# Performance work log

Measured on AMD Instinct MI355X. Metric: run time of the kernel, lower is better.

## Reference

```python
import jax, jax.numpy as jnp
import numpy as np

H, DQ, DK, DV, DM = 16, 64, 64, 64, 1024
NEG = -1.0e12


def setup_inputs() -> dict:
    key = jax.random.key(0)
    ks = jax.random.split(key, 16)
    B, S = 4, 1024
    s = 0.02
    inp = {
        "query": jax.random.normal(ks[0], (B, S, DM), jnp.float32),
        "key": jax.random.normal(ks[1], (B, S, DM), jnp.float32),
        "value": jax.random.normal(ks[2], (B, S, DM), jnp.float32),
        "mask": jax.random.randint(ks[3], (B, S), 0, 2, jnp.int32),
        "Wq": jax.random.normal(ks[4], (H * DQ, DM), jnp.float32) * s,
        "bq": jnp.zeros((H * DQ,), jnp.float32),
        "Wk": jax.random.normal(ks[5], (H * DK, DM), jnp.float32) * s,
        "bk": jnp.zeros((H * DK,), jnp.float32),
        "Wv": jax.random.normal(ks[6], (H * DV, DM), jnp.float32) * s,
        "bv": jnp.zeros((H * DV,), jnp.float32),
        "Wo": jax.random.normal(ks[7], (DM, H * DV), jnp.float32) * s,
        "bo": jnp.zeros((DM,), jnp.float32),
        "ln_g": jnp.ones((DM,), jnp.float32),
        "ln_b": jnp.zeros((DM,), jnp.float32),
    }
    return inp


def _attention(query, key, value, mask, Wq, bq, Wk, bk, Wv, bv, Wo, bo, ln_g, ln_b):
    B, qL, _ = query.shape
    kL = key.shape[1]
    mf = mask.astype(jnp.float32)  # [B, kL] ; 1 = masked token
    # padding mask broadcast over query rows, then self-attn: masked query rows fully masked
    m = jnp.broadcast_to(mf[:, None, :], (B, qL, kL))
    m = jnp.where(mf[:, :, None] > 0, 1.0, m)  # [B, q, k]

    def proj(x, W, b, d):
        # [B,S,DM] -> [H,B,S,d]
        return (x @ W.T + b).reshape(B, -1, H, d).transpose(2, 0, 1, 3)

    q = proj(query, Wq, bq, DQ)
    k = proj(key, Wk, bk, DK)
    v = proj(value, Wv, bv, DV)

    scores = jnp.einsum("hbqd,hbkd->hbqk", q, k) / np.float32(np.sqrt(DK))
    fut = jnp.triu(jnp.ones((qL, kL), jnp.float32), k=1)  # [q,k] future mask
    scores = scores + m[None] * NEG + fut[None, None] * NEG
    attn = jax.nn.softmax(scores, axis=-1)
    attn = attn * (1.0 - m[None]) * (1.0 - fut[None, None])

    out = jnp.einsum("hbqk,hbkd->hbqd", attn, v)  # [H,B,q,DV]
    out = out.transpose(1, 2, 0, 3).reshape(B, qL, H * DV)
    out = out @ Wo.T + bo + query  # residual
    mu = jnp.mean(out, axis=-1, keepdims=True)
    var = jnp.mean(jnp.square(out - mu), axis=-1, keepdims=True)
    out = (out - mu) * jax.lax.rsqrt(var + 1e-12) * ln_g + ln_b
    return out, attn.reshape(H * B, qL, kL)


def reference(query, key, value, mask, Wq, bq, Wk, bk, Wv, bv, Wo, bo, ln_g, ln_b):
    return _attention(query, key, value, mask, Wq, bq, Wk, bk, Wv, bv, Wo, bo, ln_g, ln_b)
```

## Files before the change

kernel.cpp:

```cpp
#include <hip/hip_runtime.h>
#include <hip/hip_bf16.h>

typedef __attribute__((ext_vector_type(4))) float f32x4;
typedef __attribute__((ext_vector_type(4))) float fv4;
typedef __attribute__((ext_vector_type(8))) short bf16x8;
typedef __attribute__((ext_vector_type(4))) short bf16x4;

#define DEVI __device__ __forceinline__

constexpr int BATCH = 4, SEQ = 1024, NH = 16, HD = 64, DM_ = 1024;
constexpr int NTOK = BATCH * SEQ;

DEVI unsigned short f2bf(float f) {
  union { float f; unsigned u; } v; v.f = f;
  unsigned r = v.u + 0x7FFFu + ((v.u >> 16) & 1u);
  return (unsigned short)(r >> 16);
}

DEVI int swz64(int row, int col) {
  int byte = (row * 64 + col) * 2;
  byte ^= (row & 7) << 4;
  return byte >> 1;
}

DEVI void gld_lds16(const unsigned short* g, unsigned short* l) {
  __builtin_amdgcn_global_load_lds(
      (const __attribute__((address_space(1))) unsigned int*)g,
      (__attribute__((address_space(3))) unsigned int*)l, 16, 0, 0);
}

__global__ __launch_bounds__(256) void k_cvt(
    const float* __restrict__ q, const float* __restrict__ k,
    const float* __restrict__ v,
    const float* __restrict__ wq, const float* __restrict__ wk,
    const float* __restrict__ wv, const float* __restrict__ wo,
    unsigned short* __restrict__ Xb, unsigned short* __restrict__ Wb)
{
  const int a = blockIdx.y;
  const float* src;
  unsigned short* dst;
  int n;
  if (a < 3) {
    src = (a == 0) ? q : (a == 1) ? k : v;
    dst = Xb + (size_t)a * NTOK * DM_;
    n = NTOK * DM_;
  } else {
    src = (a == 3) ? wq : (a == 4) ? wk : (a == 5) ? wv : wo;
    dst = Wb + (size_t)(a - 3) * DM_ * DM_;
    n = DM_ * DM_;
  }
  const int idx = (blockIdx.x * 256 + threadIdx.x) * 8;
  if (idx >= n) return;
  fv4 v0 = *(const fv4*)(src + idx);
  fv4 v1 = *(const fv4*)(src + idx + 4);
  bf16x8 o;
  o[0] = (short)f2bf(v0[0]); o[1] = (short)f2bf(v0[1]);
  o[2] = (short)f2bf(v0[2]); o[3] = (short)f2bf(v0[3]);
  o[4] = (short)f2bf(v1[0]); o[5] = (short)f2bf(v1[1]);
  o[6] = (short)f2bf(v1[2]); o[7] = (short)f2bf(v1[3]);
  *(bf16x8*)(dst + idx) = o;
}

__global__ __launch_bounds__(256, 3) void k_proj(
    const unsigned short* __restrict__ Xb, const unsigned short* __restrict__ Wb,
    const float* __restrict__ bq, const float* __restrict__ bk,
    const float* __restrict__ bv,
    unsigned short* __restrict__ qo, unsigned short* __restrict__ ko,
    unsigned short* __restrict__ vTo)
{
  const int lid = blockIdx.x;
  const int wg = (lid & 7) * 96 + (lid >> 3);
  const int m0 = (wg & 31) * 128;
  const int o0g = (wg >> 5) * 128;
  const int z = o0g >> 10;
  const int o0 = o0g & 1023;

  const unsigned short* X = Xb + (size_t)z * NTOK * DM_;
  const float* bias = (z == 0) ? bq : (z == 1) ? bk : bv;

  __shared__ __align__(16) unsigned short Al[128 * 64];
  __shared__ __align__(16) unsigned short Bl[128 * 64];

  const int tid = threadIdx.x;
  const int lane = tid & 63;
  const int w = tid >> 6;
  const int wm = w & 1, wn = w >> 1;
  const int l15 = lane & 15, lg = lane >> 4;

  const int rseg = lane >> 3;
  const int cg = (lane & 7) ^ rseg;

  f32x4 acc[4][4];
#pragma unroll
  for (int i = 0; i < 4; ++i)
#pragma unroll
    for (int j = 0; j < 4; ++j) acc[i][j] = f32x4{0.f, 0.f, 0.f, 0.f};

  for (int kt = 0; kt < 16; ++kt) {
    const int k0 = kt * 64;
    __syncthreads();
#pragma unroll
    for (int i = 0; i < 4; ++i) {
      const int seg = w * 4 + i;
      const int row = seg * 8 + rseg;
      gld_lds16(X + (size_t)(m0 + row) * DM_ + k0 + cg * 8, &Al[seg * 512]);
      gld_lds16(Wb + (size_t)(o0g + row) * DM_ + k0 + cg * 8, &Bl[seg * 512]);
    }
    __syncthreads();
#pragma unroll
    for (int kk = 0; kk < 2; ++kk) {
      bf16x8 af[4], bfm[4];
#pragma unroll
      for (int m = 0; m < 4; ++m)
        af[m] = *(const bf16x8*)&Al[swz64(wm * 64 + m * 16 + l15, kk * 32 + lg * 8)];
#pragma unroll
      for (int n = 0; n < 4; ++n)
        bfm[n] = *(const bf16x8*)&Bl[swz64(wn * 64 + n * 16 + l15, kk * 32 + lg * 8)];
#pragma unroll
      for (int m = 0; m < 4; ++m)
#pragma unroll
        for (int n = 0; n < 4; ++n)
          acc[m][n] = __builtin_amdgcn_mfma_f32_16x16x32_bf16(af[m], bfm[n], acc[m][n], 0, 0, 0);
    }
  }

#pragma unroll
  for (int n = 0; n < 4; ++n) {
    const int colg = o0 + wn * 64 + n * 16 + l15;
    const float bb = bias[colg];
#pragma unroll
    for (int m = 0; m < 4; ++m) {
      const int rbase = m0 + wm * 64 + m * 16 + lg * 4;
      if (z == 2) {
        bf16x4 pv;
#pragma unroll
        for (int j = 0; j < 4; ++j) pv[j] = (short)f2bf(acc[m][n][j] + bb);
        *(bf16x4*)&vTo[((size_t)(rbase >> 10) * 1024 + colg) * 1024 + (rbase & 1023)] = pv;
      } else {
        unsigned short* Y = (z == 0) ? qo : ko;
        const float sc = (z == 0) ? 0.125f : 1.f;
#pragma unroll
        for (int j = 0; j < 4; ++j)
          Y[(size_t)(rbase + j) * DM_ + colg] = f2bf((acc[m][n][j] + bb) * sc);
      }
    }
  }
}

__global__ __launch_bounds__(512, 2) void k_attn_pv(
    const unsigned short* __restrict__ qb, const unsigned short* __restrict__ kb,
    const unsigned short* __restrict__ vT, const int* __restrict__ mask,
    float* __restrict__ attn, unsigned short* __restrict__ Ob)
{
  const int tid = threadIdx.x;
  const int lane = tid & 63;
  const int w = tid >> 6;
  const int l15 = lane & 15, lg = lane >> 4;
  const int hb = blockIdx.y;
  const int h = hb >> 2, b = hb & 3;
  const int bx = blockIdx.x;
  const int q0 = bx * 32;

  __shared__ __align__(16) unsigned short Pl[32 * 1024];
  __shared__ float red[8][2][16];

  int qglob[2];
  qglob[0] = q0 + l15;
  qglob[1] = q0 + 16 + l15;

  bf16x8 qf[2][2];
#pragma unroll
  for (int g = 0; g < 2; ++g) {
    const unsigned short* qp = qb + (size_t)(b * SEQ + qglob[g]) * DM_ + h * HD + lg * 8;
    qf[g][0] = *(const bf16x8*)qp;
    qf[g][1] = *(const bf16x8*)(qp + 32);
  }
  int qm[2];
  qm[0] = mask[b * SEQ + qglob[0]];
  qm[1] = mask[b * SEQ + qglob[1]];

  const int tt = 2 * bx + 1;
  const int ni = (tt >= w) ? ((tt - w) >> 3) + 1 : 0;

  bf16x8 kf[8][2];
#pragma unroll
  for (int i = 0; i < 8; ++i) {
    if (i < ni) {
      const int krow = (w + 8 * i) * 16 + l15;
      const unsigned short* kp = kb + (size_t)(b * SEQ + krow) * DM_ + h * HD + lg * 8;
      kf[i][0] = *(const bf16x8*)kp;
      kf[i][1] = *(const bf16x8*)(kp + 32);
    }
  }

  f32x4 acc[8][2];
#pragma unroll
  for (int i = 0; i < 8; ++i)
#pragma unroll
    for (int g = 0; g < 2; ++g) acc[i][g] = f32x4{0.f, 0.f, 0.f, 0.f};

#pragma unroll
  for (int i = 0; i < 8; ++i) {
    if (i < ni) {
#pragma unroll
      for (int g = 0; g < 2; ++g) {
        acc[i][g] = __builtin_amdgcn_mfma_f32_16x16x32_bf16(kf[i][0], qf[g][0], acc[i][g], 0, 0, 0);
        acc[i][g] = __builtin_amdgcn_mfma_f32_16x16x32_bf16(kf[i][1], qf[g][1], acc[i][g], 0, 0, 0);
      }
    }
  }

  unsigned kvb = 0;
#pragma unroll
  for (int i = 0; i < 8; ++i) {
    if (i < ni) {
      const int kbase = (w + 8 * i) * 16 + lg * 4;
      int4 mv = *(const int4*)&mask[b * SEQ + kbase];
      if (mv.x == 0) kvb |= 1u << (i * 4 + 0);
      if (mv.y == 0) kvb |= 1u << (i * 4 + 1);
      if (mv.z == 0) kvb |= 1u << (i * 4 + 2);
      if (mv.w == 0) kvb |= 1u << (i * 4 + 3);
    }
  }

  float s[2] = {0.f, 0.f};
#pragma unroll
  for (int i = 0; i < 8; ++i) {
    if (i < ni) {
      const int kbase = (w + 8 * i) * 16 + lg * 4;
#pragma unroll
      for (int j = 0; j < 4; ++j) {
        const bool kok = (kvb >> (i * 4 + j)) & 1u;
#pragma unroll
        for (int g = 0; g < 2; ++g) {
          const bool vld = kok && (qm[g] == 0) && (kbase + j <= qglob[g]);
          const float p = vld ? __expf(acc[i][g][j]) : 0.f;
          acc[i][g][j] = p;
          s[g] += p;
        }
      }
    }
  }
#pragma unroll
  for (int g = 0; g < 2; ++g) {
    s[g] += __shfl_xor(s[g], 16, 64);
    s[g] += __shfl_xor(s[g], 32, 64);
  }
  if (lane < 16) { red[w][0][l15] = s[0]; red[w][1][l15] = s[1]; }
  __syncthreads();
  float rinv[2];
#pragma unroll
  for (int g = 0; g < 2; ++g) {
    float sm = 0.f;
#pragma unroll
    for (int ww = 0; ww < 8; ++ww) sm += red[ww][g][l15];
    rinv[g] = (sm > 0.f) ? (1.f / sm) : 0.f;
  }

#pragma unroll
  for (int i = 0; i < 8; ++i) {
    const int kbase = (w + 8 * i) * 16 + lg * 4;
#pragma unroll
    for (int g = 0; g < 2; ++g) {
      float* ap = attn + (size_t)hb * SEQ * SEQ + (size_t)qglob[g] * SEQ;
      fv4 st = fv4{0.f, 0.f, 0.f, 0.f};
      bf16x4 pb = bf16x4{0, 0, 0, 0};
      if (i < ni) {
#pragma unroll
        for (int j = 0; j < 4; ++j) {
          st[j] = acc[i][g][j] * rinv[g];
          pb[j] = (short)f2bf(acc[i][g][j]);
        }
      }
      __builtin_nontemporal_store(st, (fv4*)&ap[kbase]);
      const int row = g * 16 + l15;
      const int pbyte = ((row * 1024 + kbase) * 2) ^ ((l15 & 7) << 4);
      *(bf16x4*)((char*)Pl + pbyte) = pb;
    }
  }
  __syncthreads();

  const int dt = w & 3, g = w >> 2;
  const int prow = g * 16 + l15;
  f32x4 o = f32x4{0.f, 0.f, 0.f, 0.f};
  const unsigned short* vr = vT + (size_t)(b * 1024 + h * HD + dt * 16 + l15) * 1024;
#pragma unroll 4
  for (int kt = 0; kt <= bx; ++kt) {
    const int k0 = kt * 32 + lg * 8;
    bf16x8 vf = *(const bf16x8*)(vr + k0);
    const int pbyte = ((prow * 1024 + k0) * 2) ^ ((l15 & 7) << 4);
    bf16x8 pf = *(const bf16x8*)((const char*)Pl + pbyte);
    o = __builtin_amdgcn_mfma_f32_16x16x32_bf16(vf, pf, o, 0, 0, 0);
  }

  bf16x4 ob;
#pragma unroll
  for (int j = 0; j < 4; ++j) ob[j] = (short)f2bf(o[j] * rinv[g]);
  *(bf16x4*)&Ob[(size_t)(b * SEQ + q0 + prow) * DM_ + h * HD + dt * 16 + lg * 4] = ob;
}

__global__ __launch_bounds__(256) void k_oproj(
    const unsigned short* __restrict__ Ob, const unsigned short* __restrict__ Wb,
    const float* __restrict__ bo, const float* __restrict__ query,
    float* __restrict__ preln)
{
  const unsigned short* W = Wb + (size_t)3 * DM_ * DM_;

  __shared__ __align__(16) unsigned short Al[2][64 * 64];
  __shared__ __align__(16) unsigned short Bl[2][128 * 64];

  const int tid = threadIdx.x;
  const int lane = tid & 63;
  const int w = tid >> 6;
  const int wm = w & 1, wn = w >> 1;
  const int l15 = lane & 15, lg = lane >> 4;
  const int m0 = blockIdx.x * 64;
  const int o0 = blockIdx.y * 128;

  const int rseg = lane >> 3;
  const int cg = (lane & 7) ^ rseg;

  f32x4 acc[2][4];
#pragma unroll
  for (int i = 0; i < 2; ++i)
#pragma unroll
    for (int j = 0; j < 4; ++j) acc[i][j] = f32x4{0.f, 0.f, 0.f, 0.f};

#define OPROJ_STAGE(nb, kt)                                                    \
  {                                                                            \
    const int k0_ = (kt) * 64;                                                 \
    _Pragma("unroll") for (int i = 0; i < 2; ++i) {                            \
      const int seg = w * 2 + i;                                               \
      gld_lds16(Ob + (size_t)(m0 + seg * 8 + rseg) * DM_ + k0_ + cg * 8,       \
                &Al[nb][seg * 512]);                                           \
    }                                                                          \
    _Pragma("unroll") for (int i = 0; i < 4; ++i) {                            \
      const int seg = w * 4 + i;                                               \
      gld_lds16(W + (size_t)(o0 + seg * 8 + rseg) * DM_ + k0_ + cg * 8,        \
                &Bl[nb][seg * 512]);                                           \
    }                                                                          \
  }

  OPROJ_STAGE(0, 0);
  __syncthreads();

  for (int kt = 0; kt < 16; ++kt) {
    const int cur = kt & 1;
    if (kt < 15) OPROJ_STAGE(cur ^ 1, kt + 1);
#pragma unroll
    for (int kk = 0; kk < 2; ++kk) {
      bf16x8 af[2], bfm[4];
#pragma unroll
      for (int m = 0; m < 2; ++m)
        af[m] = *(const bf16x8*)&Al[cur][swz64(wm * 32 + m * 16 + l15, kk * 32 + lg * 8)];
#pragma unroll
      for (int n = 0; n < 4; ++n)
        bfm[n] = *(const bf16x8*)&Bl[cur][swz64(wn * 64 + n * 16 + l15, kk * 32 + lg * 8)];
#pragma unroll
      for (int m = 0; m < 2; ++m)
#pragma unroll
        for (int n = 0; n < 4; ++n)
          acc[m][n] = __builtin_amdgcn_mfma_f32_16x16x32_bf16(af[m], bfm[n], acc[m][n], 0, 0, 0);
    }
    __syncthreads();
  }

#pragma unroll
  for (int n = 0; n < 4; ++n) {
    const int oc = o0 + wn * 64 + n * 16 + l15;
    const float bb = bo[oc];
#pragma unroll
    for (int m = 0; m < 2; ++m) {
      const int rbase = m0 + wm * 32 + m * 16 + lg * 4;
#pragma unroll
      for (int j = 0; j < 4; ++j) {
        const size_t idx = (size_t)(rbase + j) * DM_ + oc;
        preln[idx] = acc[m][n][j] + bb + query[idx];
      }
    }
  }
}

__global__ __launch_bounds__(256) void k_ln(
    const float* __restrict__ x, const float* __restrict__ g,
    const float* __restrict__ bta, float* __restrict__ out)
{
  const int row = blockIdx.x;
  const int tid = threadIdx.x;
  const float* xr = x + (size_t)row * DM_;
  fv4 v = *(const fv4*)(xr + tid * 4);
  float s = v[0] + v[1] + v[2] + v[3];
  float s2 = v[0] * v[0] + v[1] * v[1] + v[2] * v[2] + v[3] * v[3];
#pragma unroll
  for (int off = 1; off < 64; off <<= 1) {
    s += __shfl_xor(s, off, 64);
    s2 += __shfl_xor(s2, off, 64);
  }
  __shared__ float rs[2][4];
  const int w = tid >> 6;
  if ((tid & 63) == 0) { rs[0][w] = s; rs[1][w] = s2; }
  __syncthreads();
  s = rs[0][0] + rs[0][1] + rs[0][2] + rs[0][3];
  s2 = rs[1][0] + rs[1][1] + rs[1][2] + rs[1][3];
  const float mu = s * (1.f / 1024.f);
  const float var = s2 * (1.f / 1024.f) - mu * mu;
  const float rstd = rsqrtf(var + 1e-12f);
  fv4 gg = *(const fv4*)(g + tid * 4);
  fv4 bb = *(const fv4*)(bta + tid * 4);
  fv4 o;
#pragma unroll
  for (int j = 0; j < 4; ++j) o[j] = (v[j] - mu) * rstd * gg[j] + bb[j];
  *(fv4*)(out + (size_t)row * DM_ + tid * 4) = o;
}

extern "C" void kernel_launch(void* const* d_in, const int* in_sizes, int n_in,
                              void* d_out, int out_size, void* d_ws, size_t ws_size,
                              hipStream_t stream) {
  const float* query = (const float*)d_in[0];
  const float* key   = (const float*)d_in[1];
  const float* value = (const float*)d_in[2];
  const int*   mask  = (const int*)d_in[3];
  const float* Wq = (const float*)d_in[4];
  const float* bq = (const float*)d_in[5];
  const float* Wk = (const float*)d_in[6];
  const float* bk = (const float*)d_in[7];
  const float* Wv = (const float*)d_in[8];
  const float* bv = (const float*)d_in[9];
  const float* Wo = (const float*)d_in[10];
  const float* bo = (const float*)d_in[11];
  const float* ln_g = (const float*)d_in[12];
  const float* ln_b = (const float*)d_in[13];

  float* out  = (float*)d_out;
  float* attn = out + (size_t)NTOK * DM_;

  char* ws = (char*)d_ws;
  unsigned short* Xb = (unsigned short*)ws;
  unsigned short* Wb = Xb + (size_t)3 * NTOK * DM_;
  unsigned short* qb = Wb + (size_t)4 * DM_ * DM_;
  unsigned short* kb = qb + (size_t)NTOK * DM_;
  unsigned short* vT = kb + (size_t)NTOK * DM_;
  unsigned short* Ob = vT + (size_t)NTOK * DM_;
  float* preln = (float*)ws;

  k_cvt<<<dim3(2048, 7), 256, 0, stream>>>(query, key, value, Wq, Wk, Wv, Wo,
                                           Xb, Wb);
  k_proj<<<768, 256, 0, stream>>>(Xb, Wb, bq, bk, bv, qb, kb, vT);
  k_attn_pv<<<dim3(32, 64), 512, 0, stream>>>(qb, kb, vT, mask, attn, Ob);
  k_oproj<<<dim3(64, 8), 256, 0, stream>>>(Ob, Wb, bo, query, preln);
  k_ln<<<4096, 256, 0, stream>>>(preln, ln_g, ln_b, out);
}
```

Before: 499.1 us.

## Defer attn probability stores past PV matmul, split accumulators, raise MFMA priority

```diff
diff --git a/kernel.cpp b/kernel.cpp
--- a/kernel.cpp
+++ b/kernel.cpp
@@ -199,6 +199,7 @@
 #pragma unroll
     for (int g = 0; g < 2; ++g) acc[i][g] = f32x4{0.f, 0.f, 0.f, 0.f};
 
+  __builtin_amdgcn_s_setprio(1);
 #pragma unroll
   for (int i = 0; i < 8; ++i) {
     if (i < ni) {
@@ -209,6 +210,7 @@
       }
     }
   }
+  __builtin_amdgcn_s_setprio(0);
 
   unsigned kvb = 0;
 #pragma unroll
@@ -247,32 +249,17 @@
     s[g] += __shfl_xor(s[g], 32, 64);
   }
   if (lane < 16) { red[w][0][l15] = s[0]; red[w][1][l15] = s[1]; }
-  __syncthreads();
-  float rinv[2];
-#pragma unroll
-  for (int g = 0; g < 2; ++g) {
-    float sm = 0.f;
-#pragma unroll
-    for (int ww = 0; ww < 8; ++ww) sm += red[ww][g][l15];
-    rinv[g] = (sm > 0.f) ? (1.f / sm) : 0.f;
-  }
 
 #pragma unroll
   for (int i = 0; i < 8; ++i) {
     const int kbase = (w + 8 * i) * 16 + lg * 4;
 #pragma unroll
     for (int g = 0; g < 2; ++g) {
-      float* ap = attn + (size_t)hb * SEQ * SEQ + (size_t)qglob[g] * SEQ;
-      fv4 st = fv4{0.f, 0.f, 0.f, 0.f};
       bf16x4 pb = bf16x4{0, 0, 0, 0};
       if (i < ni) {
 #pragma unroll
-        for (int j = 0; j < 4; ++j) {
-          st[j] = acc[i][g][j] * rinv[g];
-          pb[j] = (short)f2bf(acc[i][g][j]);
-        }
-      }
-      __builtin_nontemporal_store(st, (fv4*)&ap[kbase]);
+        for (int j = 0; j < 4; ++j) pb[j] = (short)f2bf(acc[i][g][j]);
+      }
       const int row = g * 16 + l15;
       const int pbyte = ((row * 1024 + kbase) * 2) ^ ((l15 & 7) << 4);
       *(bf16x4*)((char*)Pl + pbyte) = pb;
@@ -280,23 +267,59 @@
   }
   __syncthreads();
 
+  float rinv[2];
+#pragma unroll
+  for (int g = 0; g < 2; ++g) {
+    float sm = 0.f;
+#pragma unroll
+    for (int ww = 0; ww < 8; ++ww) sm += red[ww][g][l15];
+    rinv[g] = (sm > 0.f) ? (1.f / sm) : 0.f;
+  }
+
   const int dt = w & 3, g = w >> 2;
   const int prow = g * 16 + l15;
-  f32x4 o = f32x4{0.f, 0.f, 0.f, 0.f};
+  f32x4 oA = f32x4{0.f, 0.f, 0.f, 0.f};
+  f32x4 oB = f32x4{0.f, 0.f, 0.f, 0.f};
   const unsigned short* vr = vT + (size_t)(b * 1024 + h * HD + dt * 16 + l15) * 1024;
-#pragma unroll 4
-  for (int kt = 0; kt <= bx; ++kt) {
-    const int k0 = kt * 32 + lg * 8;
-    bf16x8 vf = *(const bf16x8*)(vr + k0);
-    const int pbyte = ((prow * 1024 + k0) * 2) ^ ((l15 & 7) << 4);
-    bf16x8 pf = *(const bf16x8*)((const char*)Pl + pbyte);
-    o = __builtin_amdgcn_mfma_f32_16x16x32_bf16(vf, pf, o, 0, 0, 0);
-  }
+  __builtin_amdgcn_s_setprio(1);
+#pragma unroll 2
+  for (int kt = 0; kt <= bx; kt += 2) {
+    {
+      const int k0 = kt * 32 + lg * 8;
+      bf16x8 vf = *(const bf16x8*)(vr + k0);
+      const int pbyte = ((prow * 1024 + k0) * 2) ^ ((l15 & 7) << 4);
+      bf16x8 pf = *(const bf16x8*)((const char*)Pl + pbyte);
+      oA = __builtin_amdgcn_mfma_f32_16x16x32_bf16(vf, pf, oA, 0, 0, 0);
+    }
+    if (kt + 1 <= bx) {
+      const int k1 = (kt + 1) * 32 + lg * 8;
+      bf16x8 vf = *(const bf16x8*)(vr + k1);
+      const int pbyte = ((prow * 1024 + k1) * 2) ^ ((l15 & 7) << 4);
+      bf16x8 pf = *(const bf16x8*)((const char*)Pl + pbyte);
+      oB = __builtin_amdgcn_mfma_f32_16x16x32_bf16(vf, pf, oB, 0, 0, 0);
+    }
+  }
+  __builtin_amdgcn_s_setprio(0);
 
   bf16x4 ob;
 #pragma unroll
-  for (int j = 0; j < 4; ++j) ob[j] = (short)f2bf(o[j] * rinv[g]);
+  for (int j = 0; j < 4; ++j) ob[j] = (short)f2bf((oA[j] + oB[j]) * rinv[g]);
   *(bf16x4*)&Ob[(size_t)(b * SEQ + q0 + prow) * DM_ + h * HD + dt * 16 + lg * 4] = ob;
+
+#pragma unroll
+  for (int i = 0; i < 8; ++i) {
+    const int kbase = (w + 8 * i) * 16 + lg * 4;
+#pragma unroll
+    for (int gg = 0; gg < 2; ++gg) {
+      float* ap = attn + (size_t)hb * SEQ * SEQ + (size_t)qglob[gg] * SEQ;
+      fv4 st = fv4{0.f, 0.f, 0.f, 0.f};
+      if (i < ni) {
+#pragma unroll
+        for (int j = 0; j < 4; ++j) st[j] = acc[i][gg][j] * rinv[gg];
+      }
+      __builtin_nontemporal_store(st, (fv4*)&ap[kbase]);
+    }
+  }
 }
 
 __global__ __launch_bounds__(256) void k_oproj(
```

Result: no change. 506.7 us (+1.5%).
